# Kernel optimization log

Hardware: AMD Instinct MI355X
Metric: run time of the kernel (lower is better)

Reference implementation:

```python
import jax, jax.numpy as jnp
import numpy as np

LOG100 = float(np.log(100.0))
EPS = 1e-12  # F.normalize eps


def _l2norm(x):
    # torch.nn.functional.normalize(x, dim=-1): x / max(||x||_2, eps)
    n = jnp.sqrt(jnp.sum(x * x, axis=-1, keepdims=True))
    return x / jnp.maximum(n, EPS)


def setup_inputs() -> dict:
    key = jax.random.key(0)
    k1, k2, k3, k4, k5 = jax.random.split(key, 5)
    B_, nH, N, d = 256, 8, 256, 64
    q = jax.random.normal(k1, (B_, nH, N, d), dtype=jnp.float32)
    k = jax.random.normal(k2, (B_, nH, N, d), dtype=jnp.float32)
    v = jax.random.normal(k3, (B_, nH, N, d), dtype=jnp.float32)
    logit_scale = jax.random.normal(k4, (nH, 1, 1), dtype=jnp.float32)
    bias = jax.random.normal(k5, (nH, N, N), dtype=jnp.float32)
    return {"q": q, "k": k, "v": v, "logit_scale": logit_scale, "bias": bias}


def reference(q, k, v, logit_scale, bias):
    B_, nH, N, d = q.shape
    # cosine-similarity attention (euclidean_dist=False branch)
    scores = jnp.einsum("bhnd,bhmd->bhnm", _l2norm(q), _l2norm(k))
    # attn_transform: Swin-v2-style clamped learned logit scale + rel-pos bias
    scale = jnp.exp(jnp.minimum(logit_scale, LOG100))  # (nH,1,1)
    scores = scores * scale[None] + bias[None]
    attn = jax.nn.softmax(scores, axis=-1)
    # attn_drop with p=0 is identity
    x = jnp.einsum("bhnm,bhmd->bhnd", attn, v)
    # reshape=True branch: x.transpose(1,2).reshape(B_, -1, H*head_dim) with H==N
    x = jnp.transpose(x, (0, 2, 1, 3)).reshape(B_, -1, N * d)  # (B_, nH, N*d)
    return x
```

## Files before the change

### kernel.cpp

```cpp
#include <hip/hip_runtime.h>

#define LOG100 4.605170185988091f
#define LOG2E  1.4426950408889634f

typedef _Float16 half8 __attribute__((ext_vector_type(8)));
typedef float f32x16 __attribute__((ext_vector_type(16)));

__global__ __launch_bounds__(256) void bias_pack(const float* __restrict__ bias,
                                                 unsigned* __restrict__ biasP) {
  __shared__ float tile[32][33];
  const int head = blockIdx.z;
  const int m0 = blockIdx.x * 32;
  const int n0 = blockIdx.y * 32;
  const float* src = bias + head * 65536;
  unsigned* dst = biasP + head * 32768;
  const int tx = threadIdx.x, ty = threadIdx.y;
#pragma unroll
  for (int i = ty; i < 32; i += 8) tile[i][tx] = src[(n0 + i) * 256 + m0 + tx];
  __syncthreads();
#pragma unroll
  for (int j = ty; j < 16; j += 8) {
    const float lo = tile[tx][2 * j] * LOG2E;
    const float hi = tile[tx][2 * j + 1] * LOG2E;
    dst[(m0 / 2 + j) * 256 + n0 + tx] =
        __builtin_bit_cast(unsigned, __builtin_amdgcn_cvt_pkrtz(lo, hi));
  }
}

template <bool USE_BT>
__global__ __launch_bounds__(512, 4) void attn_kernel(
    const float* __restrict__ q, const float* __restrict__ k, const float* __restrict__ v,
    const float* __restrict__ logit_scale, const float* __restrict__ bias,
    const unsigned* __restrict__ biasP, float* __restrict__ out) {
  __shared__ __align__(16) char smem[65536];
  _Float16* Kn = (_Float16*)smem;
  _Float16* Vt = (_Float16*)(smem + 32768);

  const int tid = threadIdx.x;
  const int wave = tid >> 6;
  const int lane = tid & 63;
  const int l31 = lane & 31;
  const int hi = lane >> 5;
  const int head = blockIdx.x;
  const int b = blockIdx.y;

  const long base = ((long)(b * 8 + head)) * (256 * 64);
  const float* qp = q + base;
  const float* kp = k + base;
  const float* vp = v + base;

  const float scale2 = __expf(fminf(logit_scale[head], LOG100)) * LOG2E;

  const int qrow = wave * 32 + l31;
  half8 qfrag[4];
  {
    float qf[4][8];
    float ssq = 0.f;
#pragma unroll
    for (int dk = 0; dk < 4; ++dk) {
      const float4 x0 = *(const float4*)(qp + qrow * 64 + dk * 16 + hi * 8);
      const float4 x1 = *(const float4*)(qp + qrow * 64 + dk * 16 + hi * 8 + 4);
      qf[dk][0] = x0.x; qf[dk][1] = x0.y; qf[dk][2] = x0.z; qf[dk][3] = x0.w;
      qf[dk][4] = x1.x; qf[dk][5] = x1.y; qf[dk][6] = x1.z; qf[dk][7] = x1.w;
      ssq += x0.x * x0.x + x0.y * x0.y + x0.z * x0.z + x0.w * x0.w;
      ssq += x1.x * x1.x + x1.y * x1.y + x1.z * x1.z + x1.w * x1.w;
    }
    ssq += __shfl_xor(ssq, 32);
    const float qinv = rsqrtf(fmaxf(ssq, 1e-24f));
#pragma unroll
    for (int dk = 0; dk < 4; ++dk)
#pragma unroll
      for (int j = 0; j < 8; ++j) qfrag[dk][j] = (_Float16)(qf[dk][j] * qinv);
  }

  {
    const int row_in = tid >> 4;
    const int seg = tid & 15;
#pragma unroll
    for (int it = 0; it < 8; ++it) {
      const int row = it * 32 + row_in;
      const float4 a = *(const float4*)(kp + row * 64 + seg * 4);
      float ss = a.x * a.x + a.y * a.y + a.z * a.z + a.w * a.w;
      ss += __shfl_xor(ss, 1);
      ss += __shfl_xor(ss, 2);
      ss += __shfl_xor(ss, 4);
      ss += __shfl_xor(ss, 8);
      const float inv = rsqrtf(fmaxf(ss, 1e-24f));
      union { _Float16 hh[4]; uint2 u; } pk4;
      pk4.hh[0] = (_Float16)(a.x * inv);
      pk4.hh[1] = (_Float16)(a.y * inv);
      pk4.hh[2] = (_Float16)(a.z * inv);
      pk4.hh[3] = (_Float16)(a.w * inv);
      char* wp = (char*)Kn + row * 128 + ((seg * 8) ^ ((row & 7) << 4));
      *(uint2*)wp = pk4.u;
    }
  }

  {
    const int r = lane >> 4;
    const int sx = lane & 15;
#pragma unroll
    for (int it = 0; it < 8; ++it) {
      const int kv0 = (wave * 8 + it) * 4;
      float4 a = *(const float4*)(vp + (kv0 + r) * 64 + sx * 4);
      float e1 = (r & 1) ? a.x : a.y;
      float g1 = __shfl_xor(e1, 16);
      float e2 = (r & 1) ? a.z : a.w;
      float g2 = __shfl_xor(e2, 16);
      if (r & 1) { a.x = g1; a.z = g2; } else { a.y = g1; a.w = g2; }
      float e3 = (r & 2) ? a.x : a.z;
      float g3 = __shfl_xor(e3, 32);
      float e4 = (r & 2) ? a.y : a.w;
      float g4 = __shfl_xor(e4, 32);
      if (r & 2) { a.x = g3; a.y = g4; } else { a.z = g3; a.w = g4; }
      const int d = 4 * sx + r;
      union { _Float16 hh[4]; uint2 u; } pk4;
      pk4.hh[0] = (_Float16)a.x;
      pk4.hh[1] = (_Float16)a.y;
      pk4.hh[2] = (_Float16)a.z;
      pk4.hh[3] = (_Float16)a.w;
      char* wp = (char*)Vt + d * 512 + ((kv0 * 2) ^ ((d & 31) << 4));
      *(uint2*)wp = pk4.u;
    }
  }

  __syncthreads();

  f32x16 o0 = {};
  f32x16 o1 = {};
  float m = -1.0e30f, lsum = 0.f;

  const unsigned* bP = USE_BT ? (biasP + head * 32768 + qrow) : nullptr;
  const float* bF = USE_BT ? nullptr : (bias + head * 65536 + qrow * 256 + 4 * hi);

  auto LOADB = [&](int c, unsigned bw[8]) {
    if (USE_BT) {
#pragma unroll
      for (int i = 0; i < 8; ++i) {
        const int kp_off = (i & 1) + 4 * (i >> 1) + 2 * hi;
        bw[i] = bP[(c * 16 + kp_off) * 256];
      }
    } else {
#pragma unroll
      for (int i = 0; i < 8; ++i) {
        const int kvr0 = 2 * ((i & 1) + 4 * (i >> 1) + 2 * hi);
        const float lo = bF[c * 32 + kvr0 - 4 * hi + ((kvr0 & 7) >= 4 ? 0 : 0)] * LOG2E;
        const float l0 = bF[c * 32 + ((2 * i) & 3) + 8 * ((2 * i) >> 2)] * LOG2E;
        const float l1 = bF[c * 32 + ((2 * i + 1) & 3) + 8 * ((2 * i + 1) >> 2)] * LOG2E;
        bw[i] = __builtin_bit_cast(unsigned, __builtin_amdgcn_cvt_pkrtz(l0, l1));
        (void)lo; (void)kvr0;
      }
    }
  };

  auto QKT = [&](int c) -> f32x16 {
    const int krow = c * 32 + l31;
    const char* kbase = (const char*)Kn + krow * 128;
    const int kmsk = (krow & 7) << 4;
    f32x16 s = {};
#pragma unroll
    for (int dk = 0; dk < 4; ++dk) {
      const half8 kf = *(const half8*)(kbase + ((dk * 32 + hi * 16) ^ kmsk));
      s = __builtin_amdgcn_mfma_f32_32x32x16_f16(kf, qfrag[dk], s, 0, 0, 0);
    }
    return s;
  };

  auto SOFTPV = [&](f32x16 s, int c, const unsigned bw[8]) {
#pragma unroll
    for (int i = 0; i < 8; ++i) {
      const _Float16* hp = (const _Float16*)&bw[i];
      s[2 * i] = fmaf(s[2 * i], scale2, (float)hp[0]);
      s[2 * i + 1] = fmaf(s[2 * i + 1], scale2, (float)hp[1]);
    }
    float m8[8];
#pragma unroll
    for (int i = 0; i < 8; ++i) m8[i] = fmaxf(s[2 * i], s[2 * i + 1]);
    float m4[4];
#pragma unroll
    for (int i = 0; i < 4; ++i) m4[i] = fmaxf(m8[2 * i], m8[2 * i + 1]);
    float mx = fmaxf(fmaxf(m4[0], m4[1]), fmaxf(m4[2], m4[3]));
    mx = fmaxf(mx, __shfl_xor(mx, 32));
    if (__any(mx > m + 8.0f)) {
      const float mnew = fmaxf(m, mx);
      const float corr = exp2f(m - mnew);
      lsum *= corr;
#pragma unroll
      for (int i = 0; i < 16; ++i) { o0[i] *= corr; o1[i] *= corr; }
      m = mnew;
    }
#pragma unroll
    for (int reg = 0; reg < 16; ++reg) s[reg] = exp2f(s[reg] - m);
    float a8[8];
#pragma unroll
    for (int i = 0; i < 8; ++i) a8[i] = s[2 * i] + s[2 * i + 1];
    float a4[4];
#pragma unroll
    for (int i = 0; i < 4; ++i) a4[i] = a8[2 * i] + a8[2 * i + 1];
    float psum = (a4[0] + a4[1]) + (a4[2] + a4[3]);
    psum += __shfl_xor(psum, 32);
    lsum += psum;
    unsigned pk[8];
#pragma unroll
    for (int i = 0; i < 8; ++i)
      pk[i] = __builtin_bit_cast(unsigned, __builtin_amdgcn_cvt_pkrtz(s[2 * i], s[2 * i + 1]));
    const unsigned ra = __shfl_xor(hi ? pk[0] : pk[2], 32);
    const unsigned rb = __shfl_xor(hi ? pk[1] : pk[3], 32);
    const unsigned rc = __shfl_xor(hi ? pk[4] : pk[6], 32);
    const unsigned rd = __shfl_xor(hi ? pk[5] : pk[7], 32);
    union { unsigned u[4]; half8 hh; } f0, f1;
    f0.u[0] = hi ? ra : pk[0];
    f0.u[1] = hi ? rb : pk[1];
    f0.u[2] = hi ? pk[2] : ra;
    f0.u[3] = hi ? pk[3] : rb;
    f1.u[0] = hi ? rc : pk[4];
    f1.u[1] = hi ? rd : pk[5];
    f1.u[2] = hi ? pk[6] : rc;
    f1.u[3] = hi ? pk[7] : rd;
    {
      const int d = l31;
      const char* vbase = (const char*)Vt + d * 512;
      const int msk = (d & 31) << 4;
      const half8 vf0 = *(const half8*)(vbase + ((c * 64 + hi * 16) ^ msk));
      const half8 vf1 = *(const half8*)(vbase + ((c * 64 + 32 + hi * 16) ^ msk));
      o0 = __builtin_amdgcn_mfma_f32_32x32x16_f16(vf0, f0.hh, o0, 0, 0, 0);
      o0 = __builtin_amdgcn_mfma_f32_32x32x16_f16(vf1, f1.hh, o0, 0, 0, 0);
    }
    {
      const int d = 32 + l31;
      const char* vbase = (const char*)Vt + d * 512;
      const int msk = (d & 31) << 4;
      const half8 vf0 = *(const half8*)(vbase + ((c * 64 + hi * 16) ^ msk));
      const half8 vf1 = *(const half8*)(vbase + ((c * 64 + 32 + hi * 16) ^ msk));
      o1 = __builtin_amdgcn_mfma_f32_32x32x16_f16(vf0, f0.hh, o1, 0, 0, 0);
      o1 = __builtin_amdgcn_mfma_f32_32x32x16_f16(vf1, f1.hh, o1, 0, 0, 0);
    }
  };

  unsigned bwA[8], bwB[8];
  LOADB(0, bwA);
  f32x16 sA = QKT(0);
#pragma unroll
  for (int cc = 0; cc < 4; ++cc) {
    LOADB(2 * cc + 1, bwB);
    f32x16 sB = QKT(2 * cc + 1);
    SOFTPV(sA, 2 * cc, bwA);
    if (cc < 3) {
      LOADB(2 * cc + 2, bwA);
      sA = QKT(2 * cc + 2);
    }
    SOFTPV(sB, 2 * cc + 1, bwB);
  }

  __syncthreads();

  char* ob = (char*)smem + wave * 4096;
  const float invl = 1.0f / lsum;
#pragma unroll
  for (int r = 0; r < 16; r += 2) {
    const int d0 = (r & 3) + 8 * (r >> 2) + 4 * hi;
    const unsigned w0 =
        __builtin_bit_cast(unsigned, __builtin_amdgcn_cvt_pkrtz(o0[r] * invl, o0[r + 1] * invl));
    *(unsigned*)(ob + l31 * 128 + ((d0 * 2) ^ ((l31 & 15) << 3))) = w0;
    const unsigned w1 =
        __builtin_bit_cast(unsigned, __builtin_amdgcn_cvt_pkrtz(o1[r] * invl, o1[r + 1] * invl));
    *(unsigned*)(ob + l31 * 128 + (((d0 + 32) * 2) ^ ((l31 & 15) << 3))) = w1;
  }
  __asm__ __volatile__("s_waitcnt lgkmcnt(0)" ::: "memory");
  __builtin_amdgcn_sched_barrier(0);
  const int sx = lane & 15;
  const int rr = lane >> 4;
#pragma unroll
  for (int kq = 0; kq < 8; ++kq) {
    const int qq = kq * 4 + rr;
    union { uint2 u; _Float16 hh[4]; } rd4;
    rd4.u = *(const uint2*)(ob + qq * 128 + ((sx * 8) ^ ((qq & 15) << 3)));
    float4 val;
    val.x = (float)rd4.hh[0];
    val.y = (float)rd4.hh[1];
    val.z = (float)rd4.hh[2];
    val.w = (float)rd4.hh[3];
    *(float4*)(out + (((long)(b * 256 + wave * 32 + qq) * 8 + head) * 64 + 4 * sx)) = val;
  }
}

extern "C" void kernel_launch(void* const* d_in, const int* in_sizes, int n_in,
                              void* d_out, int out_size, void* d_ws, size_t ws_size,
                              hipStream_t stream) {
  (void)in_sizes; (void)n_in; (void)out_size;
  const float* q = (const float*)d_in[0];
  const float* k = (const float*)d_in[1];
  const float* v = (const float*)d_in[2];
  const float* ls = (const float*)d_in[3];
  const float* bias = (const float*)d_in[4];
  float* out = (float*)d_out;
  const size_t bpBytes = (size_t)8 * 128 * 256 * 4;
  if (ws_size >= bpBytes) {
    unsigned* biasP = (unsigned*)d_ws;
    bias_pack<<<dim3(8, 8, 8), dim3(32, 8), 0, stream>>>(bias, biasP);
    attn_kernel<true><<<dim3(8, 256), dim3(512), 0, stream>>>(q, k, v, ls, bias, biasP, out);
  } else {
    attn_kernel<false><<<dim3(8, 256), dim3(512), 0, stream>>>(q, k, v, ls, bias, nullptr, out);
  }
}
```

Measured before the change: 146.4 us.

## Prefetch bias two chunks ahead and defer cross-half softmax reductions

The loop over key chunks changes from pairing QK^T computations to a sequential schedule. Bias words are now loaded two chunks ahead, and empty asm uses keep the next chunk's loads in flight. The per-chunk cross-lane shuffle for the row sum is removed and done once after the loop. The max shuffle now runs only inside the rescale branch. Together these cut shuffle traffic and hide bias load latency, but the sequential QK^T loses some MFMA/softmax overlap and the deeper prefetch uses more registers.

```diff
diff --git a/kernel.cpp b/kernel.cpp
--- a/kernel.cpp
+++ b/kernel.cpp
@@ -143,12 +143,9 @@
     } else {
 #pragma unroll
       for (int i = 0; i < 8; ++i) {
-        const int kvr0 = 2 * ((i & 1) + 4 * (i >> 1) + 2 * hi);
-        const float lo = bF[c * 32 + kvr0 - 4 * hi + ((kvr0 & 7) >= 4 ? 0 : 0)] * LOG2E;
         const float l0 = bF[c * 32 + ((2 * i) & 3) + 8 * ((2 * i) >> 2)] * LOG2E;
         const float l1 = bF[c * 32 + ((2 * i + 1) & 3) + 8 * ((2 * i + 1) >> 2)] * LOG2E;
         bw[i] = __builtin_bit_cast(unsigned, __builtin_amdgcn_cvt_pkrtz(l0, l1));
-        (void)lo; (void)kvr0;
       }
     }
   };
@@ -179,9 +176,9 @@
     float m4[4];
 #pragma unroll
     for (int i = 0; i < 4; ++i) m4[i] = fmaxf(m8[2 * i], m8[2 * i + 1]);
-    float mx = fmaxf(fmaxf(m4[0], m4[1]), fmaxf(m4[2], m4[3]));
-    mx = fmaxf(mx, __shfl_xor(mx, 32));
-    if (__any(mx > m + 8.0f)) {
+    const float mxl = fmaxf(fmaxf(m4[0], m4[1]), fmaxf(m4[2], m4[3]));
+    if (__any(mxl > m + 8.0f)) {
+      const float mx = fmaxf(mxl, __shfl_xor(mxl, 32));
       const float mnew = fmaxf(m, mx);
       const float corr = exp2f(m - mnew);
       lsum *= corr;
@@ -197,9 +194,7 @@
     float a4[4];
 #pragma unroll
     for (int i = 0; i < 4; ++i) a4[i] = a8[2 * i] + a8[2 * i + 1];
-    float psum = (a4[0] + a4[1]) + (a4[2] + a4[3]);
-    psum += __shfl_xor(psum, 32);
-    lsum += psum;
+    lsum += (a4[0] + a4[1]) + (a4[2] + a4[3]);
     unsigned pk[8];
 #pragma unroll
     for (int i = 0; i < 8; ++i)
@@ -237,23 +232,23 @@
     }
   };
 
-  unsigned bwA[8], bwB[8];
-  LOADB(0, bwA);
-  f32x16 sA = QKT(0);
-#pragma unroll
-  for (int cc = 0; cc < 4; ++cc) {
-    LOADB(2 * cc + 1, bwB);
-    f32x16 sB = QKT(2 * cc + 1);
-    SOFTPV(sA, 2 * cc, bwA);
-    if (cc < 3) {
-      LOADB(2 * cc + 2, bwA);
-      sA = QKT(2 * cc + 2);
-    }
-    SOFTPV(sB, 2 * cc + 1, bwB);
+  unsigned bw[8][8];
+  LOADB(0, bw[0]);
+  LOADB(1, bw[1]);
+#pragma unroll
+  for (int c = 0; c < 8; ++c) {
+    if (c + 2 < 8) LOADB(c + 2, bw[c + 2]);
+    f32x16 s = QKT(c);
+    if (c + 1 < 8) {
+#pragma unroll
+      for (int i = 0; i < 8; ++i) __asm__ __volatile__("" ::"v"(bw[c + 1][i]));
+    }
+    SOFTPV(s, c, bw[c]);
   }
 
   __syncthreads();
 
+  lsum += __shfl_xor(lsum, 32);
   char* ob = (char*)smem + wave * 4096;
   const float invl = 1.0f / lsum;
 #pragma unroll
```

After: 186.4 us. 27.3% more time.
